# Performance work log

Hardware: AMD Instinct MI355X
Metric: run time of the kernel (lower is better)

Reference implementation:

```python
import jax, jax.numpy as jnp
import numpy as np

D_MODEL = 1024
NUM_HEADS = 16
HEAD_DIM = D_MODEL // NUM_HEADS
SCALE = HEAD_DIM ** -0.5
B, N = 4, 2048


def setup_inputs() -> dict:
    key = jax.random.key(0)
    ks = jax.random.split(key, 6)
    x = jax.random.normal(ks[0], (B, N, D_MODEL), dtype=jnp.float32)
    mask = jnp.ones((B, 1, N, N), dtype=jnp.int32)
    alibi_bias = jax.random.normal(ks[1], (1, NUM_HEADS, N, N), dtype=jnp.float32)
    s = 1.0 / np.sqrt(D_MODEL)
    Wq = jax.random.normal(ks[2], (D_MODEL, D_MODEL), dtype=jnp.float32) * s
    Wk = jax.random.normal(ks[3], (D_MODEL, D_MODEL), dtype=jnp.float32) * s
    Wv = jax.random.normal(ks[4], (D_MODEL, D_MODEL), dtype=jnp.float32) * s
    Wo = jax.random.normal(ks[5], (D_MODEL, D_MODEL), dtype=jnp.float32) * s
    return {"x": x, "mask": mask, "alibi_bias": alibi_bias,
            "Wq": Wq, "Wk": Wk, "Wv": Wv, "Wo": Wo}


def reference(x, mask, alibi_bias, Wq, Wk, Wv, Wo):
    Bx, Nx, D = x.shape
    H, Hd = NUM_HEADS, HEAD_DIM
    # torch Linear(bias=False): y = x @ W.T
    q = (x @ Wq.T).reshape(Bx, Nx, H, Hd).transpose(0, 2, 1, 3)  # [B,H,N,Hd]
    k = (x @ Wk.T).reshape(Bx, Nx, H, Hd).transpose(0, 2, 1, 3)
    v = (x @ Wv.T).reshape(Bx, Nx, H, Hd).transpose(0, 2, 1, 3)
    attn = jnp.einsum('bhqd,bhkd->bhqk', q, k) * SCALE
    attn = attn + alibi_bias
    neg_inf = jnp.finfo(attn.dtype).min
    attn = jnp.where(mask == 0, neg_inf, attn)
    attn = jax.nn.softmax(attn, axis=-1)
    out = jnp.einsum('bhqk,bhkd->bhqd', attn, v)  # [B,H,N,Hd]
    out = out.transpose(0, 2, 1, 3).reshape(Bx, Nx, D)
    return out @ Wo.T
```

## Files before the change

### kernel.cpp

```cpp
#include <hip/hip_runtime.h>

#define NSEQ 2048
#define DMODEL 1024
#define NHEAD 16
#define HDIM 64
#define NBATCH 4
#define MTOT 8192
#define ATT_SCALE 0.125f
#define LOG2E 1.4426950408889634f

typedef __bf16 bf16x8 __attribute__((ext_vector_type(8)));
typedef __bf16 bf16x4 __attribute__((ext_vector_type(4)));
typedef float f32x4 __attribute__((ext_vector_type(4)));
typedef unsigned int u32x4 __attribute__((ext_vector_type(4)));
typedef unsigned short u16;
typedef unsigned int u32;
typedef unsigned long long u64;

__device__ __forceinline__ u16 f2bf(float f) {
  u32 u = __builtin_bit_cast(u32, f);
  return (u16)((u + 0x7fffu + ((u >> 16) & 1u)) >> 16);
}

__device__ __forceinline__ void gload_lds16(const void* g, void* l) {
  __builtin_amdgcn_global_load_lds(
      (__attribute__((address_space(1))) const u32*)g,
      (__attribute__((address_space(3))) u32*)l, 16, 0, 0);
}

__global__ __launch_bounds__(256) void cast_f32_bf16(const float* __restrict__ in,
                                                     u16* __restrict__ out, int n) {
  int i = (blockIdx.x * 256 + threadIdx.x) * 4;
  if (i >= n) return;
  float4 v = *(const float4*)(in + i);
  ushort4 o;
  o.x = f2bf(v.x); o.y = f2bf(v.y); o.z = f2bf(v.z); o.w = f2bf(v.w);
  *(ushort4*)(out + i) = o;
}

__global__ __launch_bounds__(256) void pack_mask(const int* __restrict__ mask,
                                                 u64* __restrict__ bits) {
  int wave = (blockIdx.x * 256 + threadIdx.x) >> 6;
  int lane = threadIdx.x & 63;
  const int* row = mask + (size_t)wave * NSEQ;
  u64* out = bits + (size_t)wave * 32;
  for (int c = 0; c < 32; ++c) {
    int v = row[c * 64 + lane];
    u64 bl = __ballot(v != 0);
    if (lane == 0) out[c] = bl;
  }
}

template <int MODE>
__global__ __launch_bounds__(256) void gemm_bt(const u16* __restrict__ A,
                                               const u16* __restrict__ W,
                                               void* __restrict__ C) {
  __shared__ __align__(16) u16 Al[128 * 64];
  __shared__ __align__(16) u16 Bl[128 * 64];
  const int tid = threadIdx.x;
  const int w = tid >> 6, l = tid & 63;
  const int l15 = l & 15, l4 = l >> 4;
  const int bm = blockIdx.x, bn = blockIdx.y;
  const int wm = w >> 1, wn = w & 1;

  f32x4 acc[4][4] = {};

  for (int ks = 0; ks < 1024; ks += 64) {
    __syncthreads();
#pragma unroll
    for (int c = 0; c < 4; ++c) {
      int g = w * 256 + c * 64 + l;
      int row = g >> 3, gc = g & 7;
      int sgc = gc ^ (row & 7);
      gload_lds16(A + (size_t)(bm * 128 + row) * 1024 + ks + sgc * 8, &Al[g * 8]);
      gload_lds16(W + (size_t)(bn * 128 + row) * 1024 + ks + sgc * 8, &Bl[g * 8]);
    }
    __syncthreads();
#pragma unroll
    for (int kc = 0; kc < 2; ++kc) {
      bf16x8 af[4], bfr[4];
#pragma unroll
      for (int mi = 0; mi < 4; ++mi) {
        int row = wm * 64 + mi * 16 + l15;
        int gc2 = (kc * 4 + l4) ^ (row & 7);
        af[mi] = *(const bf16x8*)&Al[row * 64 + gc2 * 8];
      }
#pragma unroll
      for (int ni = 0; ni < 4; ++ni) {
        int row = wn * 64 + ni * 16 + l15;
        int gc2 = (kc * 4 + l4) ^ (row & 7);
        bfr[ni] = *(const bf16x8*)&Bl[row * 64 + gc2 * 8];
      }
#pragma unroll
      for (int mi = 0; mi < 4; ++mi)
#pragma unroll
        for (int ni = 0; ni < 4; ++ni)
          acc[mi][ni] = __builtin_amdgcn_mfma_f32_16x16x32_bf16(af[mi], bfr[ni],
                                                                acc[mi][ni], 0, 0, 0);
    }
  }

#pragma unroll
  for (int mi = 0; mi < 4; ++mi)
#pragma unroll
    for (int ni = 0; ni < 4; ++ni)
#pragma unroll
      for (int r = 0; r < 4; ++r) {
        int m = bm * 128 + wm * 64 + mi * 16 + l4 * 4 + r;
        int n = bn * 128 + wn * 64 + ni * 16 + l15;
        float val = acc[mi][ni][r];
        if constexpr (MODE == 0) {
          int b = m >> 11, row = m & 2047, h = n >> 6, d = n & 63;
          ((u16*)C)[(((size_t)(b * 16 + h)) * NSEQ + row) * 64 + d] = f2bf(val);
        } else if constexpr (MODE == 1) {
          ((float*)C)[(size_t)m * 1024 + n] = val;
        } else {
          int b = m >> 11, kk = m & 2047, h = n >> 6, d = n & 63;
          ((u16*)C)[(((size_t)(b * 16 + h)) * 64 + d) * NSEQ + kk] = f2bf(val);
        }
      }
}

__global__ __launch_bounds__(256, 4) void attn_kernel(
    const u16* __restrict__ q, const u16* __restrict__ k, const u16* __restrict__ vT,
    const float* __restrict__ alibi, const u64* __restrict__ mbits,
    u16* __restrict__ o) {
  __shared__ __align__(16) u16 Kl[2][64 * 64];
  __shared__ __align__(16) u16 Vl[2][64 * 64];

  const int tid = threadIdx.x, w = tid >> 6, l = tid & 63;
  const int l15 = l & 15, l4 = l >> 4;
  const int W = blockIdx.x;
  const int W2 = (W & 7) * 256 + (W >> 3);
  const int qb = W2 & 31, Y = W2 >> 5;
  const int h = Y >> 2, b = Y & 3, bh = b * 16 + h;
  const int wq0 = qb * 64 + w * 16;
  const int myq = wq0 + l15;

  bf16x8 aq[2];
  {
    const u16* qrow = q + ((size_t)bh * NSEQ + myq) * 64;
    aq[0] = *(const bf16x8*)(qrow + l4 * 8);
    aq[1] = *(const bf16x8*)(qrow + 32 + l4 * 8);
  }

  const u16* kg[2]; const u16* vg[2];
#pragma unroll
  for (int c = 0; c < 2; ++c) {
    int g = w * 128 + c * 64 + l;
    int row = g >> 3, gc = g & 7, sgc = gc ^ (row & 7);
    kg[c] = k + ((size_t)bh * NSEQ + row) * 64 + sgc * 8;
    vg[c] = vT + ((size_t)bh * 64 + row) * NSEQ + sgc * 8;
  }

  const float* alp = alibi + (size_t)h * NSEQ * NSEQ + (size_t)myq * NSEQ + l4 * 4;
  const u64* mrp = mbits + ((size_t)b * NSEQ + myq) * 32;

  const int kfr[2] = { l15 * 128 + (((0 + l4) ^ (l15 & 7)) << 4),
                       l15 * 128 + (((4 + l4) ^ (l15 & 7)) << 4) };
  int voff[2][2];
#pragma unroll
  for (int c = 0; c < 2; ++c)
#pragma unroll
    for (int jh = 0; jh < 2; ++jh)
      voff[c][jh] = l15 * 128 + (((c * 4 + jh * 2 + (l4 >> 1)) ^ (l15 & 7)) << 4) +
                    (l4 & 1) * 8;

  f32x4 oacc[4] = {};
  float m_run = -3.0e38f, l_run = 0.f;

  auto stage = [&](u16* KB, u16* VB) {
#pragma unroll
    for (int c = 0; c < 2; ++c) {
      gload_lds16(kg[c], (char*)KB + (w * 128 + c * 64 + l) * 16);
      kg[c] += 4096;
      gload_lds16(vg[c], (char*)VB + (w * 128 + c * 64 + l) * 16);
      vg[c] += 64;
    }
  };

  stage(Kl[0], Vl[0]);
  __syncthreads();

  auto body = [&](const u16* KB, const u16* VB, u16* KN, u16* VN, int t, bool dost) {
    float4 al[4];
#pragma unroll
    for (int kb = 0; kb < 4; ++kb)
      al[kb] = *(const float4*)(alp + t * 64 + kb * 16);
    u64 mb = mrp[t];
    if (dost) stage(KN, VN);

    f32x4 st[4];
#pragma unroll
    for (int kb = 0; kb < 4; ++kb) {
      f32x4 z = {0.f, 0.f, 0.f, 0.f};
      st[kb] = z;
#pragma unroll
      for (int kc = 0; kc < 2; ++kc) {
        bf16x8 bk = *(const bf16x8*)((const char*)KB + kfr[kc] + kb * 2048);
        st[kb] = __builtin_amdgcn_mfma_f32_16x16x32_bf16(bk, aq[kc], st[kb], 0, 0, 0);
      }
    }

#pragma unroll
    for (int kb = 0; kb < 4; ++kb)
#pragma unroll
      for (int r = 0; r < 4; ++r)
        st[kb][r] = fmaf(st[kb][r], ATT_SCALE, al[kb][r]);
    if (!__all(mb == ~0ull)) {
#pragma unroll
      for (int kb = 0; kb < 4; ++kb)
#pragma unroll
        for (int r = 0; r < 4; ++r)
          if (!((mb >> (kb * 16 + l4 * 4 + r)) & 1)) st[kb][r] = -3.0e38f;
    }

    float m0 = fmaxf(fmaxf(st[0][0], st[0][1]), fmaxf(st[0][2], st[0][3]));
    float m1 = fmaxf(fmaxf(st[1][0], st[1][1]), fmaxf(st[1][2], st[1][3]));
    float m2 = fmaxf(fmaxf(st[2][0], st[2][1]), fmaxf(st[2][2], st[2][3]));
    float m3 = fmaxf(fmaxf(st[3][0], st[3][1]), fmaxf(st[3][2], st[3][3]));
    float tm = fmaxf(fmaxf(m0, m1), fmaxf(m2, m3));
    tm = fmaxf(tm, __shfl_xor(tm, 16));
    tm = fmaxf(tm, __shfl_xor(tm, 32));

    if (__any(tm > m_run + 4.0f)) {
      float mn = fmaxf(m_run, tm);
      float fac = exp2f((m_run - mn) * LOG2E);
      l_run *= fac;
      m_run = mn;
#pragma unroll
      for (int r = 0; r < 4; ++r) {
        float fr = __shfl(fac, l4 * 4 + r);
#pragma unroll
        for (int db = 0; db < 4; ++db) oacc[db][r] *= fr;
      }
    }

    float negm = -m_run * LOG2E;
    float p[16];
#pragma unroll
    for (int kb = 0; kb < 4; ++kb)
#pragma unroll
      for (int r = 0; r < 4; ++r)
        p[kb * 4 + r] = exp2f(fmaf(st[kb][r], LOG2E, negm));
    float s0 = (p[0] + p[1]) + (p[2] + p[3]);
    float s1 = (p[4] + p[5]) + (p[6] + p[7]);
    float s2 = (p[8] + p[9]) + (p[10] + p[11]);
    float s3 = (p[12] + p[13]) + (p[14] + p[15]);
    float ts = (s0 + s1) + (s2 + s3);
    ts += __shfl_xor(ts, 16);
    ts += __shfl_xor(ts, 32);
    l_run += ts;

    u32 Wp[8];
#pragma unroll
    for (int i = 0; i < 8; ++i)
      asm("v_cvt_pk_bf16_f32 %0, %1, %2" : "=v"(Wp[i]) : "v"(p[2 * i]), "v"(p[2 * i + 1]));

#pragma unroll
    for (int c = 0; c < 2; ++c) {
      u32x4 wv = {Wp[4 * c], Wp[4 * c + 1], Wp[4 * c + 2], Wp[4 * c + 3]};
      bf16x8 pa = __builtin_bit_cast(bf16x8, wv);
#pragma unroll
      for (int db = 0; db < 4; ++db) {
        bf16x4 v0 = *(const bf16x4*)((const char*)VB + voff[c][0] + db * 2048);
        bf16x4 v1 = *(const bf16x4*)((const char*)VB + voff[c][1] + db * 2048);
        bf16x8 bv = __builtin_shufflevector(v0, v1, 0, 1, 2, 3, 4, 5, 6, 7);
        oacc[db] = __builtin_amdgcn_mfma_f32_16x16x32_bf16(pa, bv, oacc[db], 0, 0, 0);
      }
    }
    __syncthreads();
  };

  for (int t2 = 0; t2 < 16; ++t2) {
    body(Kl[0], Vl[0], Kl[1], Vl[1], t2 * 2, true);
    body(Kl[1], Vl[1], Kl[0], Vl[0], t2 * 2 + 1, t2 < 15);
  }

#pragma unroll
  for (int r = 0; r < 4; ++r) {
    float lr = __shfl(l_run, l4 * 4 + r);
    float inv = __builtin_amdgcn_rcpf(lr);
    int qq = wq0 + l4 * 4 + r;
#pragma unroll
    for (int db = 0; db < 4; ++db) {
      int d = db * 16 + l15;
      o[((size_t)b * NSEQ + qq) * DMODEL + h * 64 + d] = f2bf(oacc[db][r] * inv);
    }
  }
}

extern "C" void kernel_launch(void* const* d_in, const int* in_sizes, int n_in,
                              void* d_out, int out_size, void* d_ws, size_t ws_size,
                              hipStream_t stream) {
  (void)in_sizes; (void)n_in; (void)out_size; (void)ws_size;
  const float* x = (const float*)d_in[0];
  const int* mask = (const int*)d_in[1];
  const float* alibi = (const float*)d_in[2];
  const float* Wq = (const float*)d_in[3];
  const float* Wk = (const float*)d_in[4];
  const float* Wv = (const float*)d_in[5];
  const float* Wo = (const float*)d_in[6];
  float* out = (float*)d_out;

  char* ws = (char*)d_ws;
  const size_t MB = 1u << 20;
  u16* xb  = (u16*)(ws + 0 * MB);
  u16* wqb = (u16*)(ws + 16 * MB);
  u16* wkb = (u16*)(ws + 18 * MB);
  u16* wvb = (u16*)(ws + 20 * MB);
  u16* wob = (u16*)(ws + 22 * MB);
  u16* qb  = (u16*)(ws + 24 * MB);
  u16* kb  = (u16*)(ws + 40 * MB);
  u16* vT  = (u16*)(ws + 56 * MB);
  u16* ob  = (u16*)(ws + 72 * MB);
  u64* mbits = (u64*)(ws + 88 * MB);

  cast_f32_bf16<<<8192, 256, 0, stream>>>(x, xb, MTOT * DMODEL);
  cast_f32_bf16<<<1024, 256, 0, stream>>>(Wq, wqb, DMODEL * DMODEL);
  cast_f32_bf16<<<1024, 256, 0, stream>>>(Wk, wkb, DMODEL * DMODEL);
  cast_f32_bf16<<<1024, 256, 0, stream>>>(Wv, wvb, DMODEL * DMODEL);
  cast_f32_bf16<<<1024, 256, 0, stream>>>(Wo, wob, DMODEL * DMODEL);
  pack_mask<<<2048, 256, 0, stream>>>(mask, mbits);

  dim3 gg(64, 8), blk(256);
  gemm_bt<0><<<gg, blk, 0, stream>>>(xb, wqb, qb);
  gemm_bt<0><<<gg, blk, 0, stream>>>(xb, wkb, kb);
  gemm_bt<2><<<gg, blk, 0, stream>>>(xb, wvb, vT);

  attn_kernel<<<2048, blk, 0, stream>>>(qb, kb, vT, alibi, mbits, ob);

  gemm_bt<1><<<gg, blk, 0, stream>>>(ob, wob, out);
}
```

Before: 384.7 us.

## Fuse QKV GEMMs and weight casts, restructure attention K/V loading and pipelining

The four weight casts become one launch, and the three projection GEMMs become a single launch that writes Q, K and transposed V according to the output column block. In the attention kernel, K rows are permuted at staging time so the V fragment can be read with one 16-byte LDS load instead of two 8-byte loads, and the alibi offsets and mask-bit indexing are remapped to match. Alibi and mask loads are software-pipelined one tile ahead, with explicit vmcnt waits and a single barrier per tile, and s_setprio brackets the MFMA sections. This cuts launch overhead, LDS instructions and sync stalls, but the hand-written waitcnt counts and the row permutation are fragile to get right.

```diff
diff --git a/kernel.cpp b/kernel.cpp
--- a/kernel.cpp
+++ b/kernel.cpp
@@ -10,7 +10,6 @@
 #define LOG2E 1.4426950408889634f
 
 typedef __bf16 bf16x8 __attribute__((ext_vector_type(8)));
-typedef __bf16 bf16x4 __attribute__((ext_vector_type(4)));
 typedef float f32x4 __attribute__((ext_vector_type(4)));
 typedef unsigned int u32x4 __attribute__((ext_vector_type(4)));
 typedef unsigned short u16;
@@ -36,6 +35,21 @@
   ushort4 o;
   o.x = f2bf(v.x); o.y = f2bf(v.y); o.z = f2bf(v.z); o.w = f2bf(v.w);
   *(ushort4*)(out + i) = o;
+}
+
+__global__ __launch_bounds__(256) void cast_w4(const float* __restrict__ a,
+                                               const float* __restrict__ b,
+                                               const float* __restrict__ c,
+                                               const float* __restrict__ d,
+                                               u16* __restrict__ out) {
+  int bid = blockIdx.x;
+  int which = bid >> 10, lb = bid & 1023;
+  const float* src = (which == 0) ? a : (which == 1) ? b : (which == 2) ? c : d;
+  int i = (lb * 256 + threadIdx.x) * 4;
+  float4 v = *(const float4*)(src + i);
+  ushort4 o;
+  o.x = f2bf(v.x); o.y = f2bf(v.y); o.z = f2bf(v.z); o.w = f2bf(v.w);
+  *(ushort4*)(out + (size_t)which * 1048576 + i) = o;
 }
 
 __global__ __launch_bounds__(256) void pack_mask(const int* __restrict__ mask,
@@ -51,10 +65,11 @@
   }
 }
 
-template <int MODE>
-__global__ __launch_bounds__(256) void gemm_bt(const u16* __restrict__ A,
-                                               const u16* __restrict__ W,
-                                               void* __restrict__ C) {
+__global__ __launch_bounds__(256) void gemm_qkv(const u16* __restrict__ A,
+                                                const u16* __restrict__ Wc,
+                                                u16* __restrict__ qo,
+                                                u16* __restrict__ ko,
+                                                u16* __restrict__ vo) {
   __shared__ __align__(16) u16 Al[128 * 64];
   __shared__ __align__(16) u16 Bl[128 * 64];
   const int tid = threadIdx.x;
@@ -73,7 +88,7 @@
       int row = g >> 3, gc = g & 7;
       int sgc = gc ^ (row & 7);
       gload_lds16(A + (size_t)(bm * 128 + row) * 1024 + ks + sgc * 8, &Al[g * 8]);
-      gload_lds16(W + (size_t)(bn * 128 + row) * 1024 + ks + sgc * 8, &Bl[g * 8]);
+      gload_lds16(Wc + (size_t)(bn * 128 + row) * 1024 + ks + sgc * 8, &Bl[g * 8]);
     }
     __syncthreads();
 #pragma unroll
@@ -100,6 +115,72 @@
     }
   }
 
+  const int which = bn >> 3;
+#pragma unroll
+  for (int mi = 0; mi < 4; ++mi)
+#pragma unroll
+    for (int ni = 0; ni < 4; ++ni)
+#pragma unroll
+      for (int r = 0; r < 4; ++r) {
+        int m = bm * 128 + wm * 64 + mi * 16 + l4 * 4 + r;
+        int n = (bn & 7) * 128 + wn * 64 + ni * 16 + l15;
+        int b = m >> 11, row = m & 2047, h = n >> 6, d = n & 63;
+        u16 val = f2bf(acc[mi][ni][r]);
+        size_t bh = (size_t)(b * 16 + h);
+        if (which == 0)      qo[(bh * NSEQ + row) * 64 + d] = val;
+        else if (which == 1) ko[(bh * NSEQ + row) * 64 + d] = val;
+        else                 vo[(bh * 64 + d) * NSEQ + row] = val;
+      }
+}
+
+__global__ __launch_bounds__(256) void gemm_out(const u16* __restrict__ A,
+                                                const u16* __restrict__ W,
+                                                float* __restrict__ C) {
+  __shared__ __align__(16) u16 Al[128 * 64];
+  __shared__ __align__(16) u16 Bl[128 * 64];
+  const int tid = threadIdx.x;
+  const int w = tid >> 6, l = tid & 63;
+  const int l15 = l & 15, l4 = l >> 4;
+  const int bm = blockIdx.x, bn = blockIdx.y;
+  const int wm = w >> 1, wn = w & 1;
+
+  f32x4 acc[4][4] = {};
+
+  for (int ks = 0; ks < 1024; ks += 64) {
+    __syncthreads();
+#pragma unroll
+    for (int c = 0; c < 4; ++c) {
+      int g = w * 256 + c * 64 + l;
+      int row = g >> 3, gc = g & 7;
+      int sgc = gc ^ (row & 7);
+      gload_lds16(A + (size_t)(bm * 128 + row) * 1024 + ks + sgc * 8, &Al[g * 8]);
+      gload_lds16(W + (size_t)(bn * 128 + row) * 1024 + ks + sgc * 8, &Bl[g * 8]);
+    }
+    __syncthreads();
+#pragma unroll
+    for (int kc = 0; kc < 2; ++kc) {
+      bf16x8 af[4], bfr[4];
+#pragma unroll
+      for (int mi = 0; mi < 4; ++mi) {
+        int row = wm * 64 + mi * 16 + l15;
+        int gc2 = (kc * 4 + l4) ^ (row & 7);
+        af[mi] = *(const bf16x8*)&Al[row * 64 + gc2 * 8];
+      }
+#pragma unroll
+      for (int ni = 0; ni < 4; ++ni) {
+        int row = wn * 64 + ni * 16 + l15;
+        int gc2 = (kc * 4 + l4) ^ (row & 7);
+        bfr[ni] = *(const bf16x8*)&Bl[row * 64 + gc2 * 8];
+      }
+#pragma unroll
+      for (int mi = 0; mi < 4; ++mi)
+#pragma unroll
+        for (int ni = 0; ni < 4; ++ni)
+          acc[mi][ni] = __builtin_amdgcn_mfma_f32_16x16x32_bf16(af[mi], bfr[ni],
+                                                                acc[mi][ni], 0, 0, 0);
+    }
+  }
+
 #pragma unroll
   for (int mi = 0; mi < 4; ++mi)
 #pragma unroll
@@ -108,16 +189,7 @@
       for (int r = 0; r < 4; ++r) {
         int m = bm * 128 + wm * 64 + mi * 16 + l4 * 4 + r;
         int n = bn * 128 + wn * 64 + ni * 16 + l15;
-        float val = acc[mi][ni][r];
-        if constexpr (MODE == 0) {
-          int b = m >> 11, row = m & 2047, h = n >> 6, d = n & 63;
-          ((u16*)C)[(((size_t)(b * 16 + h)) * NSEQ + row) * 64 + d] = f2bf(val);
-        } else if constexpr (MODE == 1) {
-          ((float*)C)[(size_t)m * 1024 + n] = val;
-        } else {
-          int b = m >> 11, kk = m & 2047, h = n >> 6, d = n & 63;
-          ((u16*)C)[(((size_t)(b * 16 + h)) * 64 + d) * NSEQ + kk] = f2bf(val);
-        }
+        C[(size_t)m * 1024 + n] = acc[mi][ni][r];
       }
 }
 
@@ -149,22 +221,16 @@
   for (int c = 0; c < 2; ++c) {
     int g = w * 128 + c * 64 + l;
     int row = g >> 3, gc = g & 7, sgc = gc ^ (row & 7);
-    kg[c] = k + ((size_t)bh * NSEQ + row) * 64 + sgc * 8;
+    int srow = (row & 0x23) | (((row >> 2) & 3) << 3) | (((row >> 4) & 1) << 2);
+    kg[c] = k + ((size_t)bh * NSEQ + srow) * 64 + sgc * 8;
     vg[c] = vT + ((size_t)bh * 64 + row) * NSEQ + sgc * 8;
   }
 
-  const float* alp = alibi + (size_t)h * NSEQ * NSEQ + (size_t)myq * NSEQ + l4 * 4;
+  const float* alp = alibi + (size_t)h * NSEQ * NSEQ + (size_t)myq * NSEQ + 8 * l4;
   const u64* mrp = mbits + ((size_t)b * NSEQ + myq) * 32;
 
   const int kfr[2] = { l15 * 128 + (((0 + l4) ^ (l15 & 7)) << 4),
                        l15 * 128 + (((4 + l4) ^ (l15 & 7)) << 4) };
-  int voff[2][2];
-#pragma unroll
-  for (int c = 0; c < 2; ++c)
-#pragma unroll
-    for (int jh = 0; jh < 2; ++jh)
-      voff[c][jh] = l15 * 128 + (((c * 4 + jh * 2 + (l4 >> 1)) ^ (l15 & 7)) << 4) +
-                    (l4 & 1) * 8;
 
   f32x4 oacc[4] = {};
   float m_run = -3.0e38f, l_run = 0.f;
@@ -179,17 +245,33 @@
     }
   };
 
+  auto loadal = [&](float4* a, u64& m, int t) {
+    a[0] = *(const float4*)(alp + t * 64);
+    a[1] = *(const float4*)(alp + t * 64 + 4);
+    a[2] = *(const float4*)(alp + t * 64 + 32);
+    a[3] = *(const float4*)(alp + t * 64 + 36);
+    m = mrp[t];
+  };
+
+  float4 alA[4], alB[4];
+  u64 mbA, mbB;
+
   stage(Kl[0], Vl[0]);
-  __syncthreads();
-
-  auto body = [&](const u16* KB, const u16* VB, u16* KN, u16* VN, int t, bool dost) {
-    float4 al[4];
-#pragma unroll
-    for (int kb = 0; kb < 4; ++kb)
-      al[kb] = *(const float4*)(alp + t * 64 + kb * 16);
-    u64 mb = mrp[t];
+  loadal(alA, mbA, 0);
+
+  auto body = [&](const u16* KB, const u16* VB, u16* KN, u16* VN,
+                  const float4* alc, u64 mbc, float4* aln, u64& mbn,
+                  int t, bool dost) {
+    if (dost) {
+      loadal(aln, mbn, t + 1);
+      asm volatile("s_waitcnt vmcnt(5)" ::: "memory");
+    } else {
+      asm volatile("s_waitcnt vmcnt(0)" ::: "memory");
+    }
+    __builtin_amdgcn_s_barrier();
     if (dost) stage(KN, VN);
 
+    __builtin_amdgcn_s_setprio(1);
     f32x4 st[4];
 #pragma unroll
     for (int kb = 0; kb < 4; ++kb) {
@@ -201,18 +283,21 @@
         st[kb] = __builtin_amdgcn_mfma_f32_16x16x32_bf16(bk, aq[kc], st[kb], 0, 0, 0);
       }
     }
+    __builtin_amdgcn_s_setprio(0);
 
 #pragma unroll
     for (int kb = 0; kb < 4; ++kb)
 #pragma unroll
       for (int r = 0; r < 4; ++r)
-        st[kb][r] = fmaf(st[kb][r], ATT_SCALE, al[kb][r]);
-    if (!__all(mb == ~0ull)) {
+        st[kb][r] = fmaf(st[kb][r], ATT_SCALE, alc[kb][r]);
+    if (!__all(mbc == ~0ull)) {
 #pragma unroll
       for (int kb = 0; kb < 4; ++kb)
 #pragma unroll
-        for (int r = 0; r < 4; ++r)
-          if (!((mb >> (kb * 16 + l4 * 4 + r)) & 1)) st[kb][r] = -3.0e38f;
+        for (int r = 0; r < 4; ++r) {
+          int bit = 32 * (kb >> 1) + 8 * l4 + 4 * (kb & 1) + r;
+          if (!((mbc >> bit) & 1)) st[kb][r] = -3.0e38f;
+        }
     }
 
     float m0 = fmaxf(fmaxf(st[0][0], st[0][1]), fmaxf(st[0][2], st[0][3]));
@@ -257,24 +342,23 @@
     for (int i = 0; i < 8; ++i)
       asm("v_cvt_pk_bf16_f32 %0, %1, %2" : "=v"(Wp[i]) : "v"(p[2 * i]), "v"(p[2 * i + 1]));
 
+    __builtin_amdgcn_s_setprio(1);
 #pragma unroll
     for (int c = 0; c < 2; ++c) {
       u32x4 wv = {Wp[4 * c], Wp[4 * c + 1], Wp[4 * c + 2], Wp[4 * c + 3]};
       bf16x8 pa = __builtin_bit_cast(bf16x8, wv);
 #pragma unroll
       for (int db = 0; db < 4; ++db) {
-        bf16x4 v0 = *(const bf16x4*)((const char*)VB + voff[c][0] + db * 2048);
-        bf16x4 v1 = *(const bf16x4*)((const char*)VB + voff[c][1] + db * 2048);
-        bf16x8 bv = __builtin_shufflevector(v0, v1, 0, 1, 2, 3, 4, 5, 6, 7);
+        bf16x8 bv = *(const bf16x8*)((const char*)VB + kfr[c] + db * 2048);
         oacc[db] = __builtin_amdgcn_mfma_f32_16x16x32_bf16(pa, bv, oacc[db], 0, 0, 0);
       }
     }
-    __syncthreads();
+    __builtin_amdgcn_s_setprio(0);
   };
 
   for (int t2 = 0; t2 < 16; ++t2) {
-    body(Kl[0], Vl[0], Kl[1], Vl[1], t2 * 2, true);
-    body(Kl[1], Vl[1], Kl[0], Vl[0], t2 * 2 + 1, t2 < 15);
+    body(Kl[0], Vl[0], Kl[1], Vl[1], alA, mbA, alB, mbB, t2 * 2, true);
+    body(Kl[1], Vl[1], Kl[0], Vl[0], alB, mbB, alA, mbA, t2 * 2 + 1, t2 < 15);
   }
 
 #pragma unroll
@@ -307,8 +391,6 @@
   const size_t MB = 1u << 20;
   u16* xb  = (u16*)(ws + 0 * MB);
   u16* wqb = (u16*)(ws + 16 * MB);
-  u16* wkb = (u16*)(ws + 18 * MB);
-  u16* wvb = (u16*)(ws + 20 * MB);
   u16* wob = (u16*)(ws + 22 * MB);
   u16* qb  = (u16*)(ws + 24 * MB);
   u16* kb  = (u16*)(ws + 40 * MB);
@@ -317,18 +399,12 @@
   u64* mbits = (u64*)(ws + 88 * MB);
 
   cast_f32_bf16<<<8192, 256, 0, stream>>>(x, xb, MTOT * DMODEL);
-  cast_f32_bf16<<<1024, 256, 0, stream>>>(Wq, wqb, DMODEL * DMODEL);
-  cast_f32_bf16<<<1024, 256, 0, stream>>>(Wk, wkb, DMODEL * DMODEL);
-  cast_f32_bf16<<<1024, 256, 0, stream>>>(Wv, wvb, DMODEL * DMODEL);
-  cast_f32_bf16<<<1024, 256, 0, stream>>>(Wo, wob, DMODEL * DMODEL);
+  cast_w4<<<4096, 256, 0, stream>>>(Wq, Wk, Wv, Wo, wqb);
   pack_mask<<<2048, 256, 0, stream>>>(mask, mbits);
 
-  dim3 gg(64, 8), blk(256);
-  gemm_bt<0><<<gg, blk, 0, stream>>>(xb, wqb, qb);
-  gemm_bt<0><<<gg, blk, 0, stream>>>(xb, wkb, kb);
-  gemm_bt<2><<<gg, blk, 0, stream>>>(xb, wvb, vT);
-
-  attn_kernel<<<2048, blk, 0, stream>>>(qb, kb, vT, alibi, mbits, ob);
-
-  gemm_bt<1><<<gg, blk, 0, stream>>>(ob, wob, out);
-}
+  gemm_qkv<<<dim3(64, 24), 256, 0, stream>>>(xb, wqb, qb, kb, vT);
+
+  attn_kernel<<<2048, 256, 0, stream>>>(qb, kb, vT, alibi, mbits, ob);
+
+  gemm_out<<<dim3(64, 8), 256, 0, stream>>>(ob, wob, out);
+}
```

Result: slower. 401.3 us (+4.3%).
